# Optimization experiments

Measured on AMD Instinct MI355X. Metric: run time of the kernel, lower is better.

## Reference

```python
import jax, jax.numpy as jnp
import numpy as np

NUM_TOKENS = 8192
EMBED_DIM = 32
BETA = 1.0
DECAY = 0.99
L2_EPS = 1e-12  # torch F.normalize denom clamp


def l2norm(t):
    return t / jnp.maximum(jnp.linalg.norm(t, axis=-1, keepdims=True), L2_EPS)


def setup_inputs() -> dict:
    key = jax.random.key(0)
    k1, k2 = jax.random.split(key)
    z = jax.random.normal(k1, (32, EMBED_DIM, 16, 16), dtype=jnp.float32)  # [B, C, H, W]
    embedding = l2norm(jax.random.normal(k2, (NUM_TOKENS, EMBED_DIM), dtype=jnp.float32))
    cluster_sizes = jnp.zeros((NUM_TOKENS,), dtype=jnp.float32)
    return {"z": z, "embedding": embedding, "cluster_sizes": cluster_sizes}


def reference(z, embedding, cluster_sizes):
    B, C, H, W = z.shape
    zc = jnp.transpose(z, (0, 2, 3, 1))          # channel_last: [B, H, W, C]
    zn = l2norm(zc)
    z_flat = zn.reshape(-1, C)                   # [N, C], N = B*H*W

    # nearest centroid by cosine similarity (codebook rows are unit norm)
    cos_sim = z_flat @ embedding.T               # [N, K]
    token_ids = jnp.argmax(cos_sim, axis=-1)     # [N]
    z_q_flat = embedding[token_ids]              # gather, [N, C]
    z_q = z_q_flat.reshape(zn.shape)

    # EMA statistics (training branch; one-hot @ matmuls expressed as scatter-adds)
    bins = jnp.zeros((NUM_TOKENS,), z.dtype).at[token_ids].add(1.0)      # encodings.sum(0)
    new_cluster_sizes = cluster_sizes * DECAY + (1.0 - DECAY) * bins
    zero_mask = bins == 0
    bins_c = jnp.where(zero_mask, 1.0, bins)
    embed_sum = jnp.zeros((NUM_TOKENS, C), z.dtype).at[token_ids].add(z_flat)  # (z_flat.T @ onehot).T
    embed_normalized = l2norm(embed_sum / bins_c[:, None])
    embed_normalized = jnp.where(zero_mask[:, None], embedding, embed_normalized)
    new_embedding = l2norm(embedding * DECAY + (1.0 - DECAY) * embed_normalized)

    # commitment loss + straight-through estimator
    loss = BETA * jnp.mean((jax.lax.stop_gradient(z_q) - zn) ** 2)
    z_q_st = zn + jax.lax.stop_gradient(z_q - zn)
    z_q_out = jnp.transpose(z_q_st, (0, 3, 1, 2))  # back to [B, C, H, W]

    return (z_q_out, loss, token_ids.reshape(B, H, W), new_embedding, new_cluster_sizes)
```

## Files before the change

kernel.cpp:

```cpp
#include <hip/hip_runtime.h>


#define NTOK   8192
#define NCODE  8192
#define CDIM   32
#define HW     256
#define DECAYF 0.99f
#define EPSF   0.01f

#define OUT_ZQ   0
#define OUT_LOSS 262144
#define OUT_IDS  262145
#define OUT_EMB  270337
#define OUT_CS   532481

#define WS_ZN     0u
#define WS_ZNBF   1048576u
#define WS_EBF    1572864u
#define WS_PMAX   2097152u
#define WS_PACK   3145728u

#define CHUNK  256
#define NCHUNK (NCODE / CHUNK)
#define TILES  (CHUNK / 16)

typedef __attribute__((ext_vector_type(8))) short bf16x8;
typedef __attribute__((ext_vector_type(4))) float f32x4;

__device__ inline unsigned short f2bf(float x) {
    unsigned u = __float_as_uint(x);
    return (unsigned short)((u + 0x7FFFu + ((u >> 16) & 1u)) >> 16);
}
__device__ inline unsigned fmap(float s) {
    unsigned u = __float_as_uint(s);
    return (u & 0x80000000u) ? ~u : (u | 0x80000000u);
}

__device__ inline void stage_chunk(const unsigned short* __restrict__ ebf,
                                   int kbase, float4* lbs5, int t) {
    const float4* src = (const float4*)(ebf + (size_t)kbase * CDIM);
#pragma unroll
    for (int j = 0; j < 4; ++j) {
        int u = t + j * 256;
        int row = u >> 2, seg = u & 3;
        lbs5[row * 5 + seg] = src[u];
    }
}

__global__ __launch_bounds__(256) void k_prep(const float* __restrict__ z,
                                              const float* __restrict__ emb,
                                              float* __restrict__ zn,
                                              unsigned short* __restrict__ znbf,
                                              unsigned short* __restrict__ ebf,
                                              unsigned long long* __restrict__ packed,
                                              float* __restrict__ out) {
    int bid = blockIdx.x, t = threadIdx.x;
    if (bid < 32) {
        int n = bid * 256 + t;
        int b = n >> 8, hw = n & 255;
        const float* zp = z + (size_t)b * (CDIM * HW) + hw;
        float v[CDIM];
        float ss = 0.f;
#pragma unroll
        for (int c = 0; c < CDIM; ++c) {
            float tv = zp[c * HW];
            v[c] = tv;
            ss += tv * tv;
        }
        float d = fmaxf(sqrtf(ss), 1e-12f);
        float* o = zn + (size_t)n * CDIM;
        unsigned short* ob = znbf + (size_t)n * CDIM;
#pragma unroll
        for (int c = 0; c < CDIM; ++c) {
            float tv = v[c] / d;
            o[c] = tv;
            ob[c] = f2bf(tv);
        }
    } else if (bid < 160) {
        int base = (bid - 32) * 2048 + t * 8;
        const float4* s = (const float4*)(emb + base);
        float4 x4 = s[0], y4 = s[1];
        ushort4 u0 = {f2bf(x4.x), f2bf(x4.y), f2bf(x4.z), f2bf(x4.w)};
        ushort4 u1 = {f2bf(y4.x), f2bf(y4.y), f2bf(y4.z), f2bf(y4.w)};
        *(ushort4*)(ebf + base) = u0;
        *(ushort4*)(ebf + base + 4) = u1;
    } else if (bid < 164) {
        int base = (bid - 160) * 2048 + t;
#pragma unroll
        for (int j = 0; j < 8; ++j) packed[base + j * 256] = 0ull;
    } else {
        if (t == 0) out[OUT_LOSS] = 0.f;
    }
}

__global__ __launch_bounds__(256) void k_max(const unsigned short* __restrict__ znbf,
                                             const unsigned short* __restrict__ ebf,
                                             float* __restrict__ pmax) {
    __shared__ float4 lbs5[CHUNK * 5];
    __shared__ float lmax[256];
    int kbase = blockIdx.y * CHUNK;
    stage_chunk(ebf, kbase, lbs5, threadIdx.x);
    __syncthreads();

    int wave = threadIdx.x >> 6, lane = threadIdx.x & 63;
    int col = lane & 15, quad = lane >> 4;
    int wtok = blockIdx.x * 256 + wave * 64;

    bf16x8 a[4];
#pragma unroll
    for (int f = 0; f < 4; ++f)
        a[f] = *(const bf16x8*)(znbf + (size_t)(wtok + f * 16 + col) * CDIM + quad * 8);

    const bf16x8* bl = (const bf16x8*)lbs5;
    const f32x4 zero4 = {0.f, 0.f, 0.f, 0.f};
    float m[4][4];
#pragma unroll
    for (int f = 0; f < 4; ++f)
#pragma unroll
        for (int r = 0; r < 4; ++r) m[f][r] = -1e30f;

    for (int t = 0; t < TILES; ++t) {
        bf16x8 b = bl[(t * 16 + col) * 5 + quad];
#pragma unroll
        for (int f = 0; f < 4; ++f) {
            f32x4 d = __builtin_amdgcn_mfma_f32_16x16x32_bf16(a[f], b, zero4, 0, 0, 0);
#pragma unroll
            for (int r = 0; r < 4; ++r) m[f][r] = fmaxf(m[f][r], d[r]);
        }
    }
#pragma unroll
    for (int f = 0; f < 4; ++f)
#pragma unroll
        for (int r = 0; r < 4; ++r) {
            float v = m[f][r];
#pragma unroll
            for (int s = 1; s < 16; s <<= 1) v = fmaxf(v, __shfl_xor(v, s));
            if (col == 0) lmax[wave * 64 + f * 16 + quad * 4 + r] = v;
        }
    __syncthreads();
    pmax[(size_t)blockIdx.y * NTOK + blockIdx.x * 256 + threadIdx.x] = lmax[threadIdx.x];
}

__global__ __launch_bounds__(256) void k_pick(const unsigned short* __restrict__ znbf,
                                              const unsigned short* __restrict__ ebf,
                                              const float* __restrict__ zn,
                                              const float* __restrict__ emb,
                                              const float* __restrict__ pmax,
                                              unsigned long long* __restrict__ packed) {
    __shared__ float4 lbs5[CHUNK * 5];
    __shared__ float lthr[256];
    int kbase = blockIdx.y * CHUNK;
    stage_chunk(ebf, kbase, lbs5, threadIdx.x);
    {
        int tok = blockIdx.x * 256 + threadIdx.x;
        float mx = -1e30f;
#pragma unroll
        for (int ch = 0; ch < NCHUNK; ++ch)
            mx = fmaxf(mx, pmax[(size_t)ch * NTOK + tok]);
        lthr[threadIdx.x] = mx - EPSF;
    }
    __syncthreads();

    int wave = threadIdx.x >> 6, lane = threadIdx.x & 63;
    int col = lane & 15, quad = lane >> 4;
    int wtok = blockIdx.x * 256 + wave * 64;

    bf16x8 a[4];
#pragma unroll
    for (int f = 0; f < 4; ++f)
        a[f] = *(const bf16x8*)(znbf + (size_t)(wtok + f * 16 + col) * CDIM + quad * 8);

    float thr[4][4];
#pragma unroll
    for (int f = 0; f < 4; ++f)
#pragma unroll
        for (int r = 0; r < 4; ++r)
            thr[f][r] = lthr[wave * 64 + f * 16 + quad * 4 + r];

    const bf16x8* bl = (const bf16x8*)lbs5;
    const f32x4 zero4 = {0.f, 0.f, 0.f, 0.f};

    for (int t = 0; t < TILES; ++t) {
        bf16x8 b = bl[(t * 16 + col) * 5 + quad];
#pragma unroll
        for (int f = 0; f < 4; ++f) {
            f32x4 d = __builtin_amdgcn_mfma_f32_16x16x32_bf16(a[f], b, zero4, 0, 0, 0);
#pragma unroll
            for (int r = 0; r < 4; ++r) {
                if (d[r] >= thr[f][r]) {
                    int tok = wtok + f * 16 + quad * 4 + r;
                    int code = kbase + t * 16 + col;
                    const float* zp = zn + (size_t)tok * CDIM;
                    const float* ep = emb + (size_t)code * CDIM;
                    float a0 = 0.f, a1 = 0.f, a2 = 0.f, a3 = 0.f;
#pragma unroll
                    for (int j = 0; j < 8; ++j) {
                        a0 = __builtin_fmaf(zp[4 * j + 0], ep[4 * j + 0], a0);
                        a1 = __builtin_fmaf(zp[4 * j + 1], ep[4 * j + 1], a1);
                        a2 = __builtin_fmaf(zp[4 * j + 2], ep[4 * j + 2], a2);
                        a3 = __builtin_fmaf(zp[4 * j + 3], ep[4 * j + 3], a3);
                    }
                    float s = (a0 + a1) + (a2 + a3);
                    atomicMax(packed + tok, ((unsigned long long)fmap(s) << 13) |
                                            (unsigned long long)(8191 - code));
                }
            }
        }
    }
}

__global__ __launch_bounds__(256) void k_final(const unsigned long long* __restrict__ packed,
                                               const float* __restrict__ zn,
                                               const float* __restrict__ emb,
                                               const float* __restrict__ cs,
                                               float* __restrict__ out) {
    __shared__ float lesum[32][32];
    __shared__ int lbins[32];
    __shared__ int lsid[32];
    __shared__ float ls4[4];

    int blk = blockIdx.x, t = threadIdx.x;
    int wave = t >> 6, lane = t & 63;
    int tok0 = blk * 32, kbase = blk * 32;

    if (t < 32) lbins[t] = 0;
#pragma unroll
    for (int i = 0; i < 4; ++i) {
        int idx = i * 256 + t;
        lesum[idx >> 5][idx & 31] = 0.f;
    }
    if (t < 32) {
        int n = tok0 + t;
        int id = 8191 - (int)(packed[n] & 8191ull);
        lsid[t] = id;
        out[OUT_IDS + n] = (float)id;
    }
    __syncthreads();

    float s = 0.f;
#pragma unroll
    for (int i = 0; i < 4; ++i) {
        int idx = i * 256 + t;
        int tl = idx >> 5, c = idx & 31;
        int n = tok0 + tl;
        int id = lsid[tl];
        float ev = emb[(size_t)id * CDIM + c];
        float zv = zn[(size_t)n * CDIM + c];
        int b = n >> 8, hw = n & 255;
        out[OUT_ZQ + ((size_t)b * CDIM + c) * HW + hw] = ev;
        float dd = ev - zv;
        s += dd * dd;
    }
#pragma unroll
    for (int off = 32; off > 0; off >>= 1) s += __shfl_down(s, off);
    if (lane == 0) ls4[wave] = s;
    __syncthreads();
    if (t == 0)
        atomicAdd(out + OUT_LOSS,
                  (ls4[0] + ls4[1] + ls4[2] + ls4[3]) * (1.0f / 262144.0f));

    for (int i = 0; i < 32; ++i) {
        int n = i * 256 + t;
        int id = 8191 - (int)(packed[n] & 8191ull);
        unsigned kl = (unsigned)(id - kbase);
        if (kl < 32u) {
            atomicAdd(&lbins[kl], 1);
            const float* zp = zn + (size_t)n * CDIM;
#pragma unroll
            for (int c = 0; c < CDIM; ++c)
                atomicAdd(&lesum[kl][c], zp[c]);
        }
    }
    __syncthreads();

#pragma unroll
    for (int i = 0; i < 4; ++i) {
        int idx = i * 256 + t;
        int kl = idx >> 5, c = idx & 31;
        int k = kbase + kl;
        int bi = lbins[kl];
        float bf = (float)bi;
        bool zero = (bi == 0);
        float tv = lesum[kl][c] / (zero ? 1.0f : bf);
        float ss = tv * tv;
#pragma unroll
        for (int sh = 1; sh < 32; sh <<= 1) ss += __shfl_xor(ss, sh);
        float d = fmaxf(sqrtf(ss), 1e-12f);
        float ew = emb[(size_t)k * CDIM + c];
        float en = zero ? ew : (tv / d);
        float w = ew * DECAYF + (1.0f - DECAYF) * en;
        float ss2 = w * w;
#pragma unroll
        for (int sh = 1; sh < 32; sh <<= 1) ss2 += __shfl_xor(ss2, sh);
        float d2 = fmaxf(sqrtf(ss2), 1e-12f);
        out[OUT_EMB + (size_t)k * CDIM + c] = w / d2;
        if (c == 0) out[OUT_CS + k] = cs[k] * DECAYF + (1.0f - DECAYF) * bf;
    }
}

extern "C" void kernel_launch(void* const* d_in, const int* in_sizes, int n_in,
                              void* d_out, int out_size, void* d_ws, size_t ws_size,
                              hipStream_t stream) {
    const float* z   = (const float*)d_in[0];
    const float* emb = (const float*)d_in[1];
    const float* cs  = (const float*)d_in[2];
    float* out = (float*)d_out;
    char* ws = (char*)d_ws;

    float* zn                  = (float*)(ws + WS_ZN);
    unsigned short* znbf       = (unsigned short*)(ws + WS_ZNBF);
    unsigned short* ebf        = (unsigned short*)(ws + WS_EBF);
    float* pmax                = (float*)(ws + WS_PMAX);
    unsigned long long* packed = (unsigned long long*)(ws + WS_PACK);

    k_prep<<<dim3(165), 256, 0, stream>>>(z, emb, zn, znbf, ebf, packed, out);
    k_max<<<dim3(NTOK / 256, NCHUNK), 256, 0, stream>>>(znbf, ebf, pmax);
    k_pick<<<dim3(NTOK / 256, NCHUNK), 256, 0, stream>>>(znbf, ebf, zn, emb, pmax, packed);
    k_final<<<dim3(256), 256, 0, stream>>>(packed, zn, emb, cs, out);
}
```

Measured before the change: 120.0 us.

## Fuse max and candidate sweep, rescore per-chunk candidates in separate pick kernel

The separate k_max and k_pick passes over the bf16 codebook are merged into one sweep. Each block finds its chunk-local max, then rescans its MFMA tiles to record up to four candidate codes within an epsilon of that local max. A new per-token kernel then rescores in fp32 only the candidates from chunks whose max is near the global max, falling back to the full chunk when candidates overflow. This removes a second full MFMA pass and the 64-bit global atomics. The costs are candidate storage traffic and a small 32-block pick kernel with serial, divergent per-thread loops.

```diff
diff --git a/kernel.cpp b/kernel.cpp
--- a/kernel.cpp
+++ b/kernel.cpp
@@ -18,11 +18,14 @@
 #define WS_ZNBF   1048576u
 #define WS_EBF    1572864u
 #define WS_PMAX   2097152u
-#define WS_PACK   3145728u
+#define WS_CCNT   3145728u
+#define WS_CAND   3407872u
+#define WS_IDS    5505024u
 
 #define CHUNK  256
 #define NCHUNK (NCODE / CHUNK)
 #define TILES  (CHUNK / 16)
+#define CANDS  4
 
 typedef __attribute__((ext_vector_type(8))) short bf16x8;
 typedef __attribute__((ext_vector_type(4))) float f32x4;
@@ -30,10 +33,6 @@
 __device__ inline unsigned short f2bf(float x) {
     unsigned u = __float_as_uint(x);
     return (unsigned short)((u + 0x7FFFu + ((u >> 16) & 1u)) >> 16);
-}
-__device__ inline unsigned fmap(float s) {
-    unsigned u = __float_as_uint(s);
-    return (u & 0x80000000u) ? ~u : (u | 0x80000000u);
 }
 
 __device__ inline void stage_chunk(const unsigned short* __restrict__ ebf,
@@ -45,6 +44,21 @@
         int row = u >> 2, seg = u & 3;
         lbs5[row * 5 + seg] = src[u];
     }
+}
+
+__device__ __forceinline__ float dot32(const float* zr, const float* __restrict__ emb,
+                                       int code) {
+    const float4* ep4 = (const float4*)(emb + (size_t)code * CDIM);
+    float a0 = 0.f, a1 = 0.f, a2 = 0.f, a3 = 0.f;
+#pragma unroll
+    for (int j = 0; j < 8; ++j) {
+        float4 e4 = ep4[j];
+        a0 = __builtin_fmaf(zr[4 * j + 0], e4.x, a0);
+        a1 = __builtin_fmaf(zr[4 * j + 1], e4.y, a1);
+        a2 = __builtin_fmaf(zr[4 * j + 2], e4.z, a2);
+        a3 = __builtin_fmaf(zr[4 * j + 3], e4.w, a3);
+    }
+    return (a0 + a1) + (a2 + a3);
 }
 
 __global__ __launch_bounds__(256) void k_prep(const float* __restrict__ z,
@@ -52,7 +66,6 @@
                                               float* __restrict__ zn,
                                               unsigned short* __restrict__ znbf,
                                               unsigned short* __restrict__ ebf,
-                                              unsigned long long* __restrict__ packed,
                                               float* __restrict__ out) {
     int bid = blockIdx.x, t = threadIdx.x;
     if (bid < 32) {
@@ -84,21 +97,21 @@
         ushort4 u1 = {f2bf(y4.x), f2bf(y4.y), f2bf(y4.z), f2bf(y4.w)};
         *(ushort4*)(ebf + base) = u0;
         *(ushort4*)(ebf + base + 4) = u1;
-    } else if (bid < 164) {
-        int base = (bid - 160) * 2048 + t;
-#pragma unroll
-        for (int j = 0; j < 8; ++j) packed[base + j * 256] = 0ull;
     } else {
         if (t == 0) out[OUT_LOSS] = 0.f;
     }
 }
 
-__global__ __launch_bounds__(256) void k_max(const unsigned short* __restrict__ znbf,
-                                             const unsigned short* __restrict__ ebf,
-                                             float* __restrict__ pmax) {
+__global__ __launch_bounds__(256) void k_sweep(const unsigned short* __restrict__ znbf,
+                                               const unsigned short* __restrict__ ebf,
+                                               float* __restrict__ pmax,
+                                               unsigned char* __restrict__ ccnt,
+                                               unsigned short* __restrict__ cand) {
     __shared__ float4 lbs5[CHUNK * 5];
     __shared__ float lmax[256];
+    __shared__ int lcnt[256];
     int kbase = blockIdx.y * CHUNK;
+    lcnt[threadIdx.x] = 0;
     stage_chunk(ebf, kbase, lbs5, threadIdx.x);
     __syncthreads();
 
@@ -136,49 +149,8 @@
 #pragma unroll
             for (int s = 1; s < 16; s <<= 1) v = fmaxf(v, __shfl_xor(v, s));
             if (col == 0) lmax[wave * 64 + f * 16 + quad * 4 + r] = v;
-        }
-    __syncthreads();
-    pmax[(size_t)blockIdx.y * NTOK + blockIdx.x * 256 + threadIdx.x] = lmax[threadIdx.x];
-}
-
-__global__ __launch_bounds__(256) void k_pick(const unsigned short* __restrict__ znbf,
-                                              const unsigned short* __restrict__ ebf,
-                                              const float* __restrict__ zn,
-                                              const float* __restrict__ emb,
-                                              const float* __restrict__ pmax,
-                                              unsigned long long* __restrict__ packed) {
-    __shared__ float4 lbs5[CHUNK * 5];
-    __shared__ float lthr[256];
-    int kbase = blockIdx.y * CHUNK;
-    stage_chunk(ebf, kbase, lbs5, threadIdx.x);
-    {
-        int tok = blockIdx.x * 256 + threadIdx.x;
-        float mx = -1e30f;
-#pragma unroll
-        for (int ch = 0; ch < NCHUNK; ++ch)
-            mx = fmaxf(mx, pmax[(size_t)ch * NTOK + tok]);
-        lthr[threadIdx.x] = mx - EPSF;
-    }
-    __syncthreads();
-
-    int wave = threadIdx.x >> 6, lane = threadIdx.x & 63;
-    int col = lane & 15, quad = lane >> 4;
-    int wtok = blockIdx.x * 256 + wave * 64;
-
-    bf16x8 a[4];
-#pragma unroll
-    for (int f = 0; f < 4; ++f)
-        a[f] = *(const bf16x8*)(znbf + (size_t)(wtok + f * 16 + col) * CDIM + quad * 8);
-
-    float thr[4][4];
-#pragma unroll
-    for (int f = 0; f < 4; ++f)
-#pragma unroll
-        for (int r = 0; r < 4; ++r)
-            thr[f][r] = lthr[wave * 64 + f * 16 + quad * 4 + r];
-
-    const bf16x8* bl = (const bf16x8*)lbs5;
-    const f32x4 zero4 = {0.f, 0.f, 0.f, 0.f};
+            m[f][r] = v - EPSF;
+        }
 
     for (int t = 0; t < TILES; ++t) {
         bf16x8 b = bl[(t * 16 + col) * 5 + quad];
@@ -187,29 +159,78 @@
             f32x4 d = __builtin_amdgcn_mfma_f32_16x16x32_bf16(a[f], b, zero4, 0, 0, 0);
 #pragma unroll
             for (int r = 0; r < 4; ++r) {
-                if (d[r] >= thr[f][r]) {
-                    int tok = wtok + f * 16 + quad * 4 + r;
-                    int code = kbase + t * 16 + col;
-                    const float* zp = zn + (size_t)tok * CDIM;
-                    const float* ep = emb + (size_t)code * CDIM;
-                    float a0 = 0.f, a1 = 0.f, a2 = 0.f, a3 = 0.f;
-#pragma unroll
-                    for (int j = 0; j < 8; ++j) {
-                        a0 = __builtin_fmaf(zp[4 * j + 0], ep[4 * j + 0], a0);
-                        a1 = __builtin_fmaf(zp[4 * j + 1], ep[4 * j + 1], a1);
-                        a2 = __builtin_fmaf(zp[4 * j + 2], ep[4 * j + 2], a2);
-                        a3 = __builtin_fmaf(zp[4 * j + 3], ep[4 * j + 3], a3);
-                    }
-                    float s = (a0 + a1) + (a2 + a3);
-                    atomicMax(packed + tok, ((unsigned long long)fmap(s) << 13) |
-                                            (unsigned long long)(8191 - code));
+                if (d[r] >= m[f][r]) {
+                    int ltok = wave * 64 + f * 16 + quad * 4 + r;
+                    int slot = atomicAdd(&lcnt[ltok], 1);
+                    if (slot < CANDS)
+                        cand[((size_t)blockIdx.y * NTOK + blockIdx.x * 256 + ltok) * CANDS + slot] =
+                            (unsigned short)(kbase + t * 16 + col);
                 }
             }
         }
     }
-}
-
-__global__ __launch_bounds__(256) void k_final(const unsigned long long* __restrict__ packed,
+    __syncthreads();
+    size_t o = (size_t)blockIdx.y * NTOK + blockIdx.x * 256 + threadIdx.x;
+    pmax[o] = lmax[threadIdx.x];
+    int c = lcnt[threadIdx.x];
+    ccnt[o] = (unsigned char)(c > 255 ? 255 : c);
+}
+
+__global__ __launch_bounds__(256) void k_pick2(const float* __restrict__ zn,
+                                               const float* __restrict__ emb,
+                                               const float* __restrict__ pmax,
+                                               const unsigned char* __restrict__ ccnt,
+                                               const unsigned long long* __restrict__ cand64,
+                                               unsigned int* __restrict__ ids,
+                                               float* __restrict__ out) {
+    int n = blockIdx.x * 256 + threadIdx.x;
+
+    float pm[NCHUNK];
+    float mx = -1e30f;
+#pragma unroll
+    for (int ch = 0; ch < NCHUNK; ++ch) {
+        pm[ch] = pmax[(size_t)ch * NTOK + n];
+        mx = fmaxf(mx, pm[ch]);
+    }
+    float thr = mx - EPSF;
+
+    float zr[CDIM];
+    const float4* zp4 = (const float4*)(zn + (size_t)n * CDIM);
+#pragma unroll
+    for (int j = 0; j < 8; ++j) {
+        float4 v4 = zp4[j];
+        zr[4 * j + 0] = v4.x;
+        zr[4 * j + 1] = v4.y;
+        zr[4 * j + 2] = v4.z;
+        zr[4 * j + 3] = v4.w;
+    }
+
+    float best = -2e30f;
+    int bcode = NCODE;
+#pragma unroll 1
+    for (int ch = 0; ch < NCHUNK; ++ch) {
+        if (pm[ch] < thr) continue;
+        int cnt = ccnt[(size_t)ch * NTOK + n];
+        if (cnt <= CANDS) {
+            unsigned long long cw = cand64[(size_t)ch * NTOK + n];
+            for (int s = 0; s < cnt; ++s) {
+                int code = (int)((cw >> (16 * s)) & 0xFFFFu);
+                float sc = dot32(zr, emb, code);
+                if (sc > best || (sc == best && code < bcode)) { best = sc; bcode = code; }
+            }
+        } else {
+            for (int c = 0; c < CHUNK; ++c) {
+                int code = ch * CHUNK + c;
+                float sc = dot32(zr, emb, code);
+                if (sc > best || (sc == best && code < bcode)) { best = sc; bcode = code; }
+            }
+        }
+    }
+    ids[n] = (unsigned int)bcode;
+    out[OUT_IDS + n] = (float)bcode;
+}
+
+__global__ __launch_bounds__(256) void k_final(const unsigned int* __restrict__ ids,
                                                const float* __restrict__ zn,
                                                const float* __restrict__ emb,
                                                const float* __restrict__ cs,
@@ -229,12 +250,7 @@
         int idx = i * 256 + t;
         lesum[idx >> 5][idx & 31] = 0.f;
     }
-    if (t < 32) {
-        int n = tok0 + t;
-        int id = 8191 - (int)(packed[n] & 8191ull);
-        lsid[t] = id;
-        out[OUT_IDS + n] = (float)id;
-    }
+    if (t < 32) lsid[t] = (int)ids[tok0 + t];
     __syncthreads();
 
     float s = 0.f;
@@ -261,7 +277,7 @@
 
     for (int i = 0; i < 32; ++i) {
         int n = i * 256 + t;
-        int id = 8191 - (int)(packed[n] & 8191ull);
+        int id = (int)ids[n];
         unsigned kl = (unsigned)(id - kbase);
         if (kl < 32u) {
             atomicAdd(&lbins[kl], 1);
@@ -311,10 +327,13 @@
     unsigned short* znbf       = (unsigned short*)(ws + WS_ZNBF);
     unsigned short* ebf        = (unsigned short*)(ws + WS_EBF);
     float* pmax                = (float*)(ws + WS_PMAX);
-    unsigned long long* packed = (unsigned long long*)(ws + WS_PACK);
-
-    k_prep<<<dim3(165), 256, 0, stream>>>(z, emb, zn, znbf, ebf, packed, out);
-    k_max<<<dim3(NTOK / 256, NCHUNK), 256, 0, stream>>>(znbf, ebf, pmax);
-    k_pick<<<dim3(NTOK / 256, NCHUNK), 256, 0, stream>>>(znbf, ebf, zn, emb, pmax, packed);
-    k_final<<<dim3(256), 256, 0, stream>>>(packed, zn, emb, cs, out);
-}
+    unsigned char* ccnt        = (unsigned char*)(ws + WS_CCNT);
+    unsigned short* cand       = (unsigned short*)(ws + WS_CAND);
+    unsigned int* ids          = (unsigned int*)(ws + WS_IDS);
+
+    k_prep<<<dim3(161), 256, 0, stream>>>(z, emb, zn, znbf, ebf, out);
+    k_sweep<<<dim3(NTOK / 256, NCHUNK), 256, 0, stream>>>(znbf, ebf, pmax, ccnt, cand);
+    k_pick2<<<dim3(NTOK / 256), 256, 0, stream>>>(zn, emb, pmax, ccnt,
+                                                  (const unsigned long long*)cand, ids, out);
+    k_final<<<dim3(256), 256, 0, stream>>>(ids, zn, emb, cs, out);
+}
```

Result: slower. 186.0 us (+54.9%).

## Replace MFMA re-pick pass with per-token exact rescan of candidate chunks

Applied to the files above, without the earlier changes.

The second bf16 MFMA pass over all codes, which used per-element threshold checks and global atomics, is replaced by a kernel that gives one wave to each token. The wave uses the per-chunk maxima to select only chunks within epsilon of the best and recomputes exact fp32 dot products for those 256 codes. A wave reduction then writes the packed best key directly, so the atomics and the zero-init of packed are no longer needed. The cost is full-chunk fp32 rescans whenever several chunks fall near the maximum, plus scattered global reads of embedding rows.

```diff
diff --git a/kernel.cpp b/kernel.cpp
--- a/kernel.cpp
+++ b/kernel.cpp
@@ -47,12 +47,26 @@
     }
 }
 
+__device__ __forceinline__ float dot32(const float* zr, const float* __restrict__ emb,
+                                       int code) {
+    const float4* ep4 = (const float4*)(emb + (size_t)code * CDIM);
+    float a0 = 0.f, a1 = 0.f, a2 = 0.f, a3 = 0.f;
+#pragma unroll
+    for (int j = 0; j < 8; ++j) {
+        float4 e4 = ep4[j];
+        a0 = __builtin_fmaf(zr[4 * j + 0], e4.x, a0);
+        a1 = __builtin_fmaf(zr[4 * j + 1], e4.y, a1);
+        a2 = __builtin_fmaf(zr[4 * j + 2], e4.z, a2);
+        a3 = __builtin_fmaf(zr[4 * j + 3], e4.w, a3);
+    }
+    return (a0 + a1) + (a2 + a3);
+}
+
 __global__ __launch_bounds__(256) void k_prep(const float* __restrict__ z,
                                               const float* __restrict__ emb,
                                               float* __restrict__ zn,
                                               unsigned short* __restrict__ znbf,
                                               unsigned short* __restrict__ ebf,
-                                              unsigned long long* __restrict__ packed,
                                               float* __restrict__ out) {
     int bid = blockIdx.x, t = threadIdx.x;
     if (bid < 32) {
@@ -84,10 +98,6 @@
         ushort4 u1 = {f2bf(y4.x), f2bf(y4.y), f2bf(y4.z), f2bf(y4.w)};
         *(ushort4*)(ebf + base) = u0;
         *(ushort4*)(ebf + base + 4) = u1;
-    } else if (bid < 164) {
-        int base = (bid - 160) * 2048 + t;
-#pragma unroll
-        for (int j = 0; j < 8; ++j) packed[base + j * 256] = 0ull;
     } else {
         if (t == 0) out[OUT_LOSS] = 0.f;
     }
@@ -141,72 +151,51 @@
     pmax[(size_t)blockIdx.y * NTOK + blockIdx.x * 256 + threadIdx.x] = lmax[threadIdx.x];
 }
 
-__global__ __launch_bounds__(256) void k_pick(const unsigned short* __restrict__ znbf,
-                                              const unsigned short* __restrict__ ebf,
-                                              const float* __restrict__ zn,
-                                              const float* __restrict__ emb,
-                                              const float* __restrict__ pmax,
-                                              unsigned long long* __restrict__ packed) {
-    __shared__ float4 lbs5[CHUNK * 5];
-    __shared__ float lthr[256];
-    int kbase = blockIdx.y * CHUNK;
-    stage_chunk(ebf, kbase, lbs5, threadIdx.x);
-    {
-        int tok = blockIdx.x * 256 + threadIdx.x;
-        float mx = -1e30f;
-#pragma unroll
-        for (int ch = 0; ch < NCHUNK; ++ch)
-            mx = fmaxf(mx, pmax[(size_t)ch * NTOK + tok]);
-        lthr[threadIdx.x] = mx - EPSF;
-    }
-    __syncthreads();
-
+__global__ __launch_bounds__(256) void k_rescan(const float* __restrict__ zn,
+                                                const float* __restrict__ emb,
+                                                const float* __restrict__ pmax,
+                                                unsigned long long* __restrict__ packed) {
     int wave = threadIdx.x >> 6, lane = threadIdx.x & 63;
-    int col = lane & 15, quad = lane >> 4;
-    int wtok = blockIdx.x * 256 + wave * 64;
-
-    bf16x8 a[4];
-#pragma unroll
-    for (int f = 0; f < 4; ++f)
-        a[f] = *(const bf16x8*)(znbf + (size_t)(wtok + f * 16 + col) * CDIM + quad * 8);
-
-    float thr[4][4];
-#pragma unroll
-    for (int f = 0; f < 4; ++f)
-#pragma unroll
-        for (int r = 0; r < 4; ++r)
-            thr[f][r] = lthr[wave * 64 + f * 16 + quad * 4 + r];
-
-    const bf16x8* bl = (const bf16x8*)lbs5;
-    const f32x4 zero4 = {0.f, 0.f, 0.f, 0.f};
-
-    for (int t = 0; t < TILES; ++t) {
-        bf16x8 b = bl[(t * 16 + col) * 5 + quad];
-#pragma unroll
-        for (int f = 0; f < 4; ++f) {
-            f32x4 d = __builtin_amdgcn_mfma_f32_16x16x32_bf16(a[f], b, zero4, 0, 0, 0);
-#pragma unroll
-            for (int r = 0; r < 4; ++r) {
-                if (d[r] >= thr[f][r]) {
-                    int tok = wtok + f * 16 + quad * 4 + r;
-                    int code = kbase + t * 16 + col;
-                    const float* zp = zn + (size_t)tok * CDIM;
-                    const float* ep = emb + (size_t)code * CDIM;
-                    float a0 = 0.f, a1 = 0.f, a2 = 0.f, a3 = 0.f;
-#pragma unroll
-                    for (int j = 0; j < 8; ++j) {
-                        a0 = __builtin_fmaf(zp[4 * j + 0], ep[4 * j + 0], a0);
-                        a1 = __builtin_fmaf(zp[4 * j + 1], ep[4 * j + 1], a1);
-                        a2 = __builtin_fmaf(zp[4 * j + 2], ep[4 * j + 2], a2);
-                        a3 = __builtin_fmaf(zp[4 * j + 3], ep[4 * j + 3], a3);
-                    }
-                    float s = (a0 + a1) + (a2 + a3);
-                    atomicMax(packed + tok, ((unsigned long long)fmap(s) << 13) |
-                                            (unsigned long long)(8191 - code));
-                }
-            }
-        }
-    }
+    int n = blockIdx.x * 4 + wave;
+
+    float pm = -1e30f;
+    if (lane < 32) pm = pmax[(size_t)lane * NTOK + n];
+    float mx = pm;
+#pragma unroll
+    for (int s = 1; s < 64; s <<= 1) mx = fmaxf(mx, __shfl_xor(mx, s));
+    float thr = mx - EPSF;
+    unsigned m32 = (unsigned)(__ballot(pm >= thr) & 0xFFFFFFFFull);
+
+    float zr[CDIM];
+    const float4* zp4 = (const float4*)(zn + (size_t)n * CDIM);
+#pragma unroll
+    for (int j = 0; j < 8; ++j) {
+        float4 v4 = zp4[j];
+        zr[4 * j + 0] = v4.x;
+        zr[4 * j + 1] = v4.y;
+        zr[4 * j + 2] = v4.z;
+        zr[4 * j + 3] = v4.w;
+    }
+
+    unsigned long long kbest = 0ull;
+    while (m32) {
+        int ch = __ffs(m32) - 1;
+        m32 &= m32 - 1;
+#pragma unroll
+        for (int j = 0; j < 4; ++j) {
+            int code = ch * CHUNK + j * 64 + lane;
+            float s = dot32(zr, emb, code);
+            unsigned long long key = ((unsigned long long)fmap(s) << 13) |
+                                     (unsigned long long)(8191 - code);
+            kbest = kbest > key ? kbest : key;
+        }
+    }
+#pragma unroll
+    for (int s = 1; s < 64; s <<= 1) {
+        unsigned long long o = __shfl_xor(kbest, s);
+        kbest = kbest > o ? kbest : o;
+    }
+    if (lane == 0) packed[n] = kbest;
 }
 
 __global__ __launch_bounds__(256) void k_final(const unsigned long long* __restrict__ packed,
@@ -313,8 +302,8 @@
     float* pmax                = (float*)(ws + WS_PMAX);
     unsigned long long* packed = (unsigned long long*)(ws + WS_PACK);
 
-    k_prep<<<dim3(165), 256, 0, stream>>>(z, emb, zn, znbf, ebf, packed, out);
+    k_prep<<<dim3(161), 256, 0, stream>>>(z, emb, zn, znbf, ebf, out);
     k_max<<<dim3(NTOK / 256, NCHUNK), 256, 0, stream>>>(znbf, ebf, pmax);
-    k_pick<<<dim3(NTOK / 256, NCHUNK), 256, 0, stream>>>(znbf, ebf, zn, emb, pmax, packed);
+    k_rescan<<<dim3(NTOK / 4), 256, 0, stream>>>(zn, emb, pmax, packed);
     k_final<<<dim3(256), 256, 0, stream>>>(packed, zn, emb, cs, out);
 }
```

Result: slower. 186.0 us (+55.0%).
